# Optimization experiments

Hardware: AMD Instinct MI355X
Metric: run time of the kernel (lower is better)

Reference implementation:

```python
import jax, jax.numpy as jnp
import numpy as np

D0 = 232          # GraphSAGE_TextMF_dyn.model_embedding_dim_origin
NUM_TRAIN = 4096  # num_train_models


def sage_conv(x, edge_index, W_l, b_l, W_r):
    """PyG SAGEConv(aggr='mean'): lin_l(mean_{j in N(i)} x_j) + lin_r(x_i)."""
    src, dst = edge_index[0], edge_index[1]
    msg = x[src]                                                    # [E, Din]
    agg = jax.ops.segment_sum(msg, dst, num_segments=x.shape[0])    # [N, Din]
    deg = jax.ops.segment_sum(jnp.ones((edge_index.shape[1],), x.dtype), dst,
                              num_segments=x.shape[0])
    agg = agg / jnp.maximum(deg, 1.0)[:, None]
    return agg @ W_l.T + b_l + x @ W_r.T


def setup_inputs() -> dict:
    key = jax.random.key(0)
    ks = jax.random.split(key, 12)
    num_models, med, hidden = 5000, 1024, 256
    num_prompts, text_dim = 100000, 768
    B, E = 16384, 131072
    s = lambda d: 1.0 / np.sqrt(d)
    return {
        "P_weight":     jax.random.normal(ks[0], (num_models, med), jnp.float32) * 0.02,
        "model_proj_W": jax.random.normal(ks[1], (D0, med), jnp.float32) * s(med),
        "model_proj_b": jnp.zeros((D0,), jnp.float32),
        "sage1_Wl":     jax.random.normal(ks[2], (hidden, D0), jnp.float32) * s(D0),
        "sage1_bl":     jnp.zeros((hidden,), jnp.float32),
        "sage1_Wr":     jax.random.normal(ks[3], (hidden, D0), jnp.float32) * s(D0),
        "sage2_Wl":     jax.random.normal(ks[4], (D0, hidden), jnp.float32) * s(hidden),
        "sage2_bl":     jnp.zeros((D0,), jnp.float32),
        "sage2_Wr":     jax.random.normal(ks[5], (D0, hidden), jnp.float32) * s(hidden),
        "Q_weight":     jax.random.normal(ks[6], (num_prompts, text_dim), jnp.float32),
        "text_proj_W":  jax.random.normal(ks[7], (D0, text_dim), jnp.float32) * s(text_dim),
        "text_proj_b":  jnp.zeros((D0,), jnp.float32),
        "cls_W":        jax.random.normal(ks[8], (2, D0), jnp.float32) * s(D0),
        "cls_b":        jnp.zeros((2,), jnp.float32),
        "edge_index":   jax.random.randint(ks[9], (2, E), 0, NUM_TRAIN),
        "model_ids":    jax.random.randint(ks[10], (B,), 0, NUM_TRAIN),
        "prompt_ids":   jax.random.randint(ks[11], (B,), 0, num_prompts),
    }


def reference(P_weight, model_proj_W, model_proj_b,
              sage1_Wl, sage1_bl, sage1_Wr,
              sage2_Wl, sage2_bl, sage2_Wr,
              Q_weight, text_proj_W, text_proj_b,
              cls_W, cls_b,
              edge_index, model_ids, prompt_ids):
    # model embedding table -> project to D0
    emb = P_weight @ model_proj_W.T + model_proj_b            # [num_models, D0]
    x = emb[:NUM_TRAIN]                                       # train models only
    # 2-layer GraphSAGE with ReLU between layers
    x = jax.nn.relu(sage_conv(x, edge_index, sage1_Wl, sage1_bl, sage1_Wr))
    x = sage_conv(x, edge_index, sage2_Wl, sage2_bl, sage2_Wr)  # [NUM_TRAIN, D0]
    # TextMF head: classifier(p * q)
    p = x[model_ids]                                          # [B, D0]
    q = Q_weight[prompt_ids] @ text_proj_W.T + text_proj_b    # [B, D0]
    return (p * q) @ cls_W.T + cls_b                          # [B, 2]
```

## Files before the change

kernel.cpp:

```cpp
#include <hip/hip_runtime.h>

#define D0 232
#define MED 1024
#define HID 256
#define TDIM 768
#define NTRAIN 4096

typedef short bf16x8 __attribute__((ext_vector_type(8)));
typedef float f32x4  __attribute__((ext_vector_type(4)));
typedef unsigned short u16;

__device__ __forceinline__ u16 f2bf(float f) {
    unsigned u = __float_as_uint(f);
    return (u16)((u + 0x7FFFu + ((u >> 16) & 1u)) >> 16);
}
__device__ __forceinline__ float bf2f(u16 h) {
    return __uint_as_float(((unsigned)h) << 16);
}
__device__ __forceinline__ void cvt8(const float4& a0, const float4& a1,
                                     bf16x8& h, bf16x8& l) {
    float f[8] = {a0.x, a0.y, a0.z, a0.w, a1.x, a1.y, a1.z, a1.w};
    #pragma unroll
    for (int i = 0; i < 8; ++i) {
        u16 hh = f2bf(f[i]);
        h[i] = (short)hh;
        l[i] = (short)f2bf(f[i] - bf2f(hh));
    }
}
__device__ __forceinline__ void cvt4(const float4 v, ushort4& h, ushort4& l) {
    h.x = f2bf(v.x); l.x = f2bf(v.x - bf2f(h.x));
    h.y = f2bf(v.y); l.y = f2bf(v.y - bf2f(h.y));
    h.z = f2bf(v.z); l.z = f2bf(v.z - bf2f(h.z));
    h.w = f2bf(v.w); l.w = f2bf(v.w - bf2f(h.w));
}

#define SROW(r, k) ((((r) ^ (k)) & 7) | ((r) & ~7))

template<int CONVA, int RELU, int EMIT, int NPASS>
__global__ __launch_bounds__(256, 2) void gemm_node(
    const float* __restrict__ A1f,
    const short* __restrict__ A1h, const short* __restrict__ A1l,
    const short* __restrict__ B1h, const short* __restrict__ B1l,
    const short* __restrict__ A2h, const short* __restrict__ A2l,
    const short* __restrict__ B2h, const short* __restrict__ B2l,
    const float* __restrict__ bias,
    float* __restrict__ Cf, u16* __restrict__ Chi, u16* __restrict__ Clo,
    int M, int N, int K)
{
    constexpr int TBM = 32;
    __shared__ short sAh[8 * TBM * 8], sAl[8 * TBM * 8];

    const int tid  = threadIdx.x;
    const int lane = tid & 63;
    const int wn   = tid >> 6;
    const int l15  = lane & 15;
    const int l4   = lane >> 4;
    const int row0 = blockIdx.y * TBM;
    const int col0 = blockIdx.x * 64;

    const int aRow  = tid >> 3;
    const int aKc   = tid & 7;
    const int aSlot = (aKc * TBM + SROW(aRow, aKc)) * 8;

    const int  colW  = col0 + wn * 16 + l15;
    const bool colOk = colW < N;
    const size_t wBase = (size_t)(colOk ? colW : 0) * K;

    const bf16x8 Z8 = {0, 0, 0, 0, 0, 0, 0, 0};
    f32x4 acc[2];
    acc[0] = (f32x4){0.f, 0.f, 0.f, 0.f};
    acc[1] = (f32x4){0.f, 0.f, 0.f, 0.f};

    for (int pass = 0; pass < NPASS; ++pass) {
        const short* Bh = pass ? B2h : B1h;
        const short* Bl = pass ? B2l : B1l;
        const short* Ah = pass ? A2h : A1h;
        const short* Al = pass ? A2l : A1l;
        const size_t aOff = (size_t)(row0 + aRow) * K;

        float4 qa0, qa1;
        bf16x8 ph, pl;

        auto loadA = [&](int k0) {
            int gk = k0 + aKc * 8;
            bool v = gk < K;
            if (CONVA && pass == 0) {
                qa0 = v ? *(const float4*)(A1f + aOff + gk)     : make_float4(0.f,0.f,0.f,0.f);
                qa1 = v ? *(const float4*)(A1f + aOff + gk + 4) : make_float4(0.f,0.f,0.f,0.f);
            } else {
                ph = v ? *(const bf16x8*)(Ah + aOff + gk) : Z8;
                pl = v ? *(const bf16x8*)(Al + aOff + gk) : Z8;
            }
        };

        loadA(0);
        for (int k0 = 0; k0 < K; k0 += 64) {
            bf16x8 bh[2], bl[2];
            #pragma unroll
            for (int ks = 0; ks < 2; ++ks) {
                int kb = k0 + (ks * 4 + l4) * 8;
                bool v = colOk && kb < K;
                bh[ks] = v ? *(const bf16x8*)(Bh + wBase + kb) : Z8;
                bl[ks] = v ? *(const bf16x8*)(Bl + wBase + kb) : Z8;
            }
            if (CONVA && pass == 0) {
                bf16x8 h, l; cvt8(qa0, qa1, h, l);
                *(bf16x8*)(sAh + aSlot) = h;
                *(bf16x8*)(sAl + aSlot) = l;
            } else {
                *(bf16x8*)(sAh + aSlot) = ph;
                *(bf16x8*)(sAl + aSlot) = pl;
            }
            __syncthreads();
            if (k0 + 64 < K) loadA(k0 + 64);

            #pragma unroll
            for (int ks = 0; ks < 2; ++ks) {
                const int pb = ks * 4 + l4;
                bf16x8 ah[2], al[2];
                #pragma unroll
                for (int m = 0; m < 2; ++m) {
                    int sl = (pb * TBM + SROW(m * 16 + l15, pb)) * 8;
                    ah[m] = *(const bf16x8*)(sAh + sl);
                    al[m] = *(const bf16x8*)(sAl + sl);
                }
                #pragma unroll
                for (int m = 0; m < 2; ++m)
                    acc[m] = __builtin_amdgcn_mfma_f32_16x16x32_bf16(ah[m], bh[ks], acc[m], 0, 0, 0);
                #pragma unroll
                for (int m = 0; m < 2; ++m)
                    acc[m] = __builtin_amdgcn_mfma_f32_16x16x32_bf16(ah[m], bl[ks], acc[m], 0, 0, 0);
                #pragma unroll
                for (int m = 0; m < 2; ++m)
                    acc[m] = __builtin_amdgcn_mfma_f32_16x16x32_bf16(al[m], bh[ks], acc[m], 0, 0, 0);
            }
            __syncthreads();
        }
    }

    if (colOk) {
        const float bv = bias[colW];
        #pragma unroll
        for (int m = 0; m < 2; ++m) {
            #pragma unroll
            for (int r = 0; r < 4; ++r) {
                int row = row0 + m * 16 + l4 * 4 + r;
                float v = acc[m][r] + bv;
                if (RELU) v = fmaxf(v, 0.0f);
                size_t idx = (size_t)row * N + colW;
                Cf[idx] = v;
                if (EMIT) {
                    u16 h = f2bf(v);
                    Chi[idx] = h;
                    Clo[idx] = f2bf(v - bf2f(h));
                }
            }
        }
    }
}

__global__ __launch_bounds__(256) void gemm_q_head(
    const float* __restrict__ Q, const int* __restrict__ prompt_ids,
    const short* __restrict__ Wh, const short* __restrict__ Wl,
    const float* __restrict__ bias,
    const float* __restrict__ x2f, const int* __restrict__ model_ids,
    const float* __restrict__ cls_W, const float* __restrict__ cls_b,
    float* __restrict__ out)
{
    constexpr int TBM = 64, K = TDIM, N = D0;
    __shared__ short sAh[8 * TBM * 8], sAl[8 * TBM * 8];
    __shared__ float hacc[TBM][2];

    const int tid  = threadIdx.x;
    const int lane = tid & 63;
    const int wn   = tid >> 6;
    const int l15  = lane & 15;
    const int l4   = lane >> 4;
    const int row0 = blockIdx.x * TBM;

    const int cid0 = tid * 2, cid1 = tid * 2 + 1;
    const int r0 = cid0 >> 3, kc0 = cid0 & 7;
    const int r1 = cid1 >> 3, kc1 = cid1 & 7;
    const int slot0 = (kc0 * TBM + SROW(r0, kc0)) * 8;
    const int slot1 = (kc1 * TBM + SROW(r1, kc1)) * 8;
    const size_t ab0 = (size_t)prompt_ids[row0 + r0] * K;
    const size_t ab1 = (size_t)prompt_ids[row0 + r1] * K;

    int colW[4]; bool cOk[4]; size_t wB[4];
    #pragma unroll
    for (int j = 0; j < 4; ++j) {
        colW[j] = wn * 64 + j * 16 + l15;
        cOk[j]  = colW[j] < N;
        wB[j]   = (size_t)(cOk[j] ? colW[j] : 0) * K;
    }

    const bf16x8 Z8 = {0, 0, 0, 0, 0, 0, 0, 0};
    f32x4 acc[4][4];
    #pragma unroll
    for (int m = 0; m < 4; ++m)
        #pragma unroll
        for (int j = 0; j < 4; ++j)
            acc[m][j] = (f32x4){0.f, 0.f, 0.f, 0.f};

    float4 qa0, qa1, qa2, qa3;
    auto loadA = [&](int k0) {
        qa0 = *(const float4*)(Q + ab0 + k0 + kc0 * 8);
        qa1 = *(const float4*)(Q + ab0 + k0 + kc0 * 8 + 4);
        qa2 = *(const float4*)(Q + ab1 + k0 + kc1 * 8);
        qa3 = *(const float4*)(Q + ab1 + k0 + kc1 * 8 + 4);
    };

    loadA(0);
    for (int k0 = 0; k0 < K; k0 += 64) {
        bf16x8 bh[2][4], bl[2][4];
        #pragma unroll
        for (int ks = 0; ks < 2; ++ks) {
            int kb = k0 + (ks * 4 + l4) * 8;
            #pragma unroll
            for (int j = 0; j < 4; ++j) {
                bh[ks][j] = cOk[j] ? *(const bf16x8*)(Wh + wB[j] + kb) : Z8;
                bl[ks][j] = cOk[j] ? *(const bf16x8*)(Wl + wB[j] + kb) : Z8;
            }
        }
        {
            bf16x8 h, l;
            cvt8(qa0, qa1, h, l);
            *(bf16x8*)(sAh + slot0) = h; *(bf16x8*)(sAl + slot0) = l;
            cvt8(qa2, qa3, h, l);
            *(bf16x8*)(sAh + slot1) = h; *(bf16x8*)(sAl + slot1) = l;
        }
        __syncthreads();
        if (k0 + 64 < K) loadA(k0 + 64);

        #pragma unroll
        for (int ks = 0; ks < 2; ++ks) {
            const int pb = ks * 4 + l4;
            bf16x8 ah[4], al[4];
            #pragma unroll
            for (int m = 0; m < 4; ++m) {
                int sl = (pb * TBM + SROW(m * 16 + l15, pb)) * 8;
                ah[m] = *(const bf16x8*)(sAh + sl);
                al[m] = *(const bf16x8*)(sAl + sl);
            }
            #pragma unroll
            for (int m = 0; m < 4; ++m)
                #pragma unroll
                for (int j = 0; j < 4; ++j)
                    acc[m][j] = __builtin_amdgcn_mfma_f32_16x16x32_bf16(ah[m], bh[ks][j], acc[m][j], 0, 0, 0);
            #pragma unroll
            for (int m = 0; m < 4; ++m)
                #pragma unroll
                for (int j = 0; j < 4; ++j)
                    acc[m][j] = __builtin_amdgcn_mfma_f32_16x16x32_bf16(ah[m], bl[ks][j], acc[m][j], 0, 0, 0);
            #pragma unroll
            for (int m = 0; m < 4; ++m)
                #pragma unroll
                for (int j = 0; j < 4; ++j)
                    acc[m][j] = __builtin_amdgcn_mfma_f32_16x16x32_bf16(al[m], bh[ks][j], acc[m][j], 0, 0, 0);
        }
        __syncthreads();
    }

    if (tid < TBM * 2) ((float*)hacc)[tid] = 0.f;
    __syncthreads();

    float bv[4], w0[4], w1[4];
    #pragma unroll
    for (int j = 0; j < 4; ++j) {
        bv[j] = cOk[j] ? bias[colW[j]]      : 0.f;
        w0[j] = cOk[j] ? cls_W[colW[j]]     : 0.f;
        w1[j] = cOk[j] ? cls_W[N + colW[j]] : 0.f;
    }

    float s0[4][4] = {}, s1[4][4] = {};
    #pragma unroll
    for (int m = 0; m < 4; ++m) {
        #pragma unroll
        for (int rr = 0; rr < 4; ++rr) {
            const int mid = model_ids[row0 + m * 16 + l4 * 4 + rr];
            const float* xr = x2f + (size_t)mid * N;
            #pragma unroll
            for (int j = 0; j < 4; ++j) {
                if (cOk[j]) {
                    float pv = (acc[m][j][rr] + bv[j]) * xr[colW[j]];
                    s0[m][rr] += pv * w0[j];
                    s1[m][rr] += pv * w1[j];
                }
            }
        }
    }
    #pragma unroll
    for (int off = 1; off < 16; off <<= 1)
        #pragma unroll
        for (int m = 0; m < 4; ++m)
            #pragma unroll
            for (int rr = 0; rr < 4; ++rr) {
                s0[m][rr] += __shfl_xor(s0[m][rr], off);
                s1[m][rr] += __shfl_xor(s1[m][rr], off);
            }
    if (l15 == 0) {
        #pragma unroll
        for (int m = 0; m < 4; ++m)
            #pragma unroll
            for (int rr = 0; rr < 4; ++rr) {
                int lr = m * 16 + l4 * 4 + rr;
                atomicAdd(&hacc[lr][0], s0[m][rr]);
                atomicAdd(&hacc[lr][1], s1[m][rr]);
            }
    }
    __syncthreads();
    if (tid < TBM * 2) {
        int r = tid >> 1, c = tid & 1;
        out[(size_t)(row0 + r) * 2 + c] = hacc[r][c] + cls_b[c];
    }
}

struct Seg  { const float* src; u16* hi; u16* lo; int n4; };
struct Segs { Seg s[6]; };

__global__ __launch_bounds__(256) void hist_conv(
    const int* __restrict__ dst, int* __restrict__ hist, int E, int HB,
    Segs segs, int total4)
{
    if ((int)blockIdx.x < HB) {
        int e = blockIdx.x * 256 + threadIdx.x;
        if (e < E) atomicAdd(&hist[dst[e]], 1);
    } else {
        int i = (blockIdx.x - HB) * 256 + threadIdx.x;
        const int stride = (gridDim.x - HB) * 256;
        for (; i < total4; i += stride) {
            int k = i, si = 0;
            while (k >= segs.s[si].n4) { k -= segs.s[si].n4; ++si; }
            float4 v = ((const float4*)segs.s[si].src)[k];
            ushort4 h, l; cvt4(v, h, l);
            ((ushort4*)segs.s[si].hi)[k] = h;
            ((ushort4*)segs.s[si].lo)[k] = l;
        }
    }
}

__global__ __launch_bounds__(1024) void scan_kernel(
    const int* __restrict__ hist, int* __restrict__ row_ptr,
    float* __restrict__ invdeg, int* __restrict__ cursor, int E)
{
    __shared__ int s[1024];
    const int t = threadIdx.x;
    int4 c = reinterpret_cast<const int4*>(hist)[t];
    int local = c.x + c.y + c.z + c.w;
    s[t] = local;
    __syncthreads();
    for (int off = 1; off < 1024; off <<= 1) {
        int v = (t >= off) ? s[t - off] : 0;
        __syncthreads();
        s[t] += v;
        __syncthreads();
    }
    int base = s[t] - local;
    row_ptr[4 * t + 0] = base;
    row_ptr[4 * t + 1] = base + c.x;
    row_ptr[4 * t + 2] = base + c.x + c.y;
    row_ptr[4 * t + 3] = base + c.x + c.y + c.z;
    if (t == 1023) row_ptr[4096] = E;
    invdeg[4 * t + 0] = 1.0f / fmaxf((float)c.x, 1.0f);
    invdeg[4 * t + 1] = 1.0f / fmaxf((float)c.y, 1.0f);
    invdeg[4 * t + 2] = 1.0f / fmaxf((float)c.z, 1.0f);
    invdeg[4 * t + 3] = 1.0f / fmaxf((float)c.w, 1.0f);
    reinterpret_cast<int4*>(cursor)[t] = make_int4(0, 0, 0, 0);
}

__global__ void scatter_kernel(
    const int* __restrict__ src, const int* __restrict__ dst,
    const int* __restrict__ row_ptr, int* __restrict__ cursor,
    int* __restrict__ csr, int E)
{
    int e = blockIdx.x * blockDim.x + threadIdx.x;
    if (e >= E) return;
    int d = dst[e];
    int pos = atomicAdd(&cursor[d], 1);
    csr[row_ptr[d] + pos] = src[e];
}

__device__ __forceinline__ void add4(float4& a, const float4 b) {
    a.x += b.x; a.y += b.y; a.z += b.z; a.w += b.w;
}

__global__ __launch_bounds__(256) void node_agg(
    const int* __restrict__ row_ptr, const int* __restrict__ csr,
    const float* __restrict__ invdeg,
    const float* __restrict__ x, u16* __restrict__ agh, u16* __restrict__ agl, int D)
{
    const int wave = threadIdx.x >> 6;
    const int lane = threadIdx.x & 63;
    const int node = blockIdx.x * 4 + wave;
    const int beg = row_ptr[node], end = row_ptr[node + 1];
    const bool act = lane < (D >> 2);
    const int fo = lane * 4;

    float4 s0 = {0,0,0,0}, s1 = {0,0,0,0}, s2 = {0,0,0,0}, s3 = {0,0,0,0};
    int j = beg;
    for (; j + 3 < end; j += 4) {
        int n0 = csr[j], n1 = csr[j + 1], n2 = csr[j + 2], n3 = csr[j + 3];
        if (act) {
            add4(s0, *(const float4*)(&x[(size_t)n0 * D + fo]));
            add4(s1, *(const float4*)(&x[(size_t)n1 * D + fo]));
            add4(s2, *(const float4*)(&x[(size_t)n2 * D + fo]));
            add4(s3, *(const float4*)(&x[(size_t)n3 * D + fo]));
        }
    }
    for (; j < end; ++j) {
        int n = csr[j];
        if (act) add4(s0, *(const float4*)(&x[(size_t)n * D + fo]));
    }
    if (act) {
        const float inv = invdeg[node];
        float4 r;
        r.x = (s0.x + s1.x + s2.x + s3.x) * inv;
        r.y = (s0.y + s1.y + s2.y + s3.y) * inv;
        r.z = (s0.z + s1.z + s2.z + s3.z) * inv;
        r.w = (s0.w + s1.w + s2.w + s3.w) * inv;
        ushort4 h, l; cvt4(r, h, l);
        *(ushort4*)(&agh[(size_t)node * D + fo]) = h;
        *(ushort4*)(&agl[(size_t)node * D + fo]) = l;
    }
}

extern "C" void kernel_launch(void* const* d_in, const int* in_sizes, int n_in,
                              void* d_out, int out_size, void* d_ws, size_t ws_size,
                              hipStream_t stream)
{
    const float* P_weight     = (const float*)d_in[0];
    const float* model_proj_W = (const float*)d_in[1];
    const float* model_proj_b = (const float*)d_in[2];
    const float* sage1_Wl     = (const float*)d_in[3];
    const float* sage1_bl     = (const float*)d_in[4];
    const float* sage1_Wr     = (const float*)d_in[5];
    const float* sage2_Wl     = (const float*)d_in[6];
    const float* sage2_bl     = (const float*)d_in[7];
    const float* sage2_Wr     = (const float*)d_in[8];
    const float* Q_weight     = (const float*)d_in[9];
    const float* text_proj_W  = (const float*)d_in[10];
    const float* text_proj_b  = (const float*)d_in[11];
    const float* cls_W        = (const float*)d_in[12];
    const float* cls_b        = (const float*)d_in[13];
    const int*   edge_index   = (const int*)d_in[14];
    const int*   model_ids    = (const int*)d_in[15];
    const int*   prompt_ids   = (const int*)d_in[16];

    const int E = in_sizes[14] / 2;
    const int B = in_sizes[15];
    const int* srcE = edge_index;
    const int* dstE = edge_index + E;

    const size_t nX0 = (size_t)NTRAIN * D0;
    const size_t nH1 = (size_t)NTRAIN * HID;
    const size_t nWp = (size_t)D0 * MED;
    const size_t nWs = (size_t)HID * D0;
    const size_t nWt = (size_t)D0 * TDIM;
    const size_t nWAll = nWp + 4 * nWs + nWt;

    float* fp  = (float*)d_ws;
    float* x0f = fp;  fp += nX0;
    float* h1f = fp;  fp += nH1;
    float* x2f = fp;  fp += nX0;
    u16* sp  = (u16*)fp;
    u16* x0h = sp;    sp += nX0;
    u16* x0l = sp;    sp += nX0;
    u16* h1h = sp;    sp += nH1;
    u16* h1l = sp;    sp += nH1;
    u16* agh = sp;    sp += nH1;
    u16* agl = sp;    sp += nH1;
    u16* Wh  = sp;    sp += nWAll;
    u16* Wl  = sp;    sp += nWAll;
    int* ib  = (int*)sp;
    int*   hist    = ib;
    int*   cursor  = ib + 4096;
    int*   row_ptr = ib + 8192;
    float* invdeg  = (float*)(ib + 12304);
    int*   csr     = ib + 16400;

    u16 *Wph = Wh,            *Wpl = Wl;
    u16 *W1lh = Wh + nWp,     *W1ll = Wl + nWp;
    u16 *W1rh = W1lh + nWs,   *W1rl = W1ll + nWs;
    u16 *W2lh = W1rh + nWs,   *W2ll = W1rl + nWs;
    u16 *W2rh = W2lh + nWs,   *W2rl = W2ll + nWs;
    u16 *Wth  = W2rh + nWs,   *Wtl  = W2rl + nWs;

    dim3 blk(256);

    hipMemsetAsync(hist, 0, 4096 * sizeof(int), stream);

    Segs segs;
    segs.s[0] = {model_proj_W, Wph,  Wpl,  (int)(nWp / 4)};
    segs.s[1] = {sage1_Wl,     W1lh, W1ll, (int)(nWs / 4)};
    segs.s[2] = {sage1_Wr,     W1rh, W1rl, (int)(nWs / 4)};
    segs.s[3] = {sage2_Wl,     W2lh, W2ll, (int)(nWs / 4)};
    segs.s[4] = {sage2_Wr,     W2rh, W2rl, (int)(nWs / 4)};
    segs.s[5] = {text_proj_W,  Wth,  Wtl,  (int)(nWt / 4)};
    const int HB = (E + 255) / 256;
    hist_conv<<<HB + 512, blk, 0, stream>>>(dstE, hist, E, HB, segs, (int)(nWAll / 4));

    scan_kernel<<<1, 1024, 0, stream>>>(hist, row_ptr, invdeg, cursor, E);
    scatter_kernel<<<(E + 255) / 256, blk, 0, stream>>>(srcE, dstE, row_ptr, cursor, csr, E);

    gemm_node<1, 0, 1, 1><<<dim3(4, NTRAIN / 32), blk, 0, stream>>>(
        P_weight, nullptr, nullptr,
        (const short*)Wph, (const short*)Wpl,
        nullptr, nullptr, nullptr, nullptr,
        model_proj_b, x0f, x0h, x0l, NTRAIN, D0, MED);

    node_agg<<<NTRAIN / 4, blk, 0, stream>>>(row_ptr, csr, invdeg, x0f, agh, agl, D0);

    gemm_node<0, 1, 1, 2><<<dim3(4, NTRAIN / 32), blk, 0, stream>>>(
        nullptr, (const short*)agh, (const short*)agl,
        (const short*)W1lh, (const short*)W1ll,
        (const short*)x0h, (const short*)x0l,
        (const short*)W1rh, (const short*)W1rl,
        sage1_bl, h1f, h1h, h1l, NTRAIN, HID, D0);

    node_agg<<<NTRAIN / 4, blk, 0, stream>>>(row_ptr, csr, invdeg, h1f, agh, agl, HID);

    gemm_node<0, 0, 0, 2><<<dim3(4, NTRAIN / 32), blk, 0, stream>>>(
        nullptr, (const short*)agh, (const short*)agl,
        (const short*)W2lh, (const short*)W2ll,
        (const short*)h1h, (const short*)h1l,
        (const short*)W2rh, (const short*)W2rl,
        sage2_bl, x2f, nullptr, nullptr, NTRAIN, D0, HID);

    gemm_q_head<<<B / 64, blk, 0, stream>>>(
        Q_weight, prompt_ids, (const short*)Wth, (const short*)Wtl,
        text_proj_b, x2f, model_ids, cls_W, cls_b, (float*)d_out);
}
```

Baseline: 168.8 us.

## Fuse hist/conv/scan via last-block pattern, fold scatter into first GEMM, shrink head tile

Histogram, weight splitting and the prefix scan now run in one kernel: the last block to finish, detected with an atomic counter, does the scan. The CSR scatter moves into the prologue of the first node GEMM, and the launch grid is flattened to 1D. The Q-head GEMM tile drops from 64 to 32 rows, doubling the block count, and gets launch bounds for two blocks per SM. The goal is fewer kernel launches and better occupancy for the head, at the cost of a serial scan inside one block and scatter work that delays the GEMM start.

```diff
diff --git a/kernel.cpp b/kernel.cpp
--- a/kernel.cpp
+++ b/kernel.cpp
@@ -36,31 +36,101 @@
 
 #define SROW(r, k) ((((r) ^ (k)) & 7) | ((r) & ~7))
 
-template<int CONVA, int RELU, int EMIT, int NPASS>
+struct Seg  { const float* src; u16* hi; u16* lo; int n4; };
+struct Segs { Seg s[6]; };
+
+__global__ __launch_bounds__(256) void k1_hist_conv_scan(
+    const int* __restrict__ dstE, int* __restrict__ hist, int E,
+    Segs segs, int total4,
+    int* __restrict__ done, int* __restrict__ row_ptr,
+    float* __restrict__ invdeg, int* __restrict__ cursor)
+{
+    const int tid  = threadIdx.x;
+    const int gidx = blockIdx.x * 256 + tid;
+    const int gstr = gridDim.x * 256;
+
+    for (int e = gidx; e < E; e += gstr)
+        atomicAdd(&hist[dstE[e]], 1);
+
+    for (int i = gidx; i < total4; i += gstr) {
+        int k = i, si = 0;
+        while (k >= segs.s[si].n4) { k -= segs.s[si].n4; ++si; }
+        float4 v = ((const float4*)segs.s[si].src)[k];
+        ushort4 h, l; cvt4(v, h, l);
+        ((ushort4*)segs.s[si].hi)[k] = h;
+        ((ushort4*)segs.s[si].lo)[k] = l;
+    }
+
+    __shared__ int amLast;
+    __syncthreads();
+    if (tid == 0)
+        amLast = (atomicAdd(done, 1) == (int)gridDim.x - 1);
+    __syncthreads();
+    if (!amLast) return;
+
+    __shared__ int s_scan[256];
+    const int base = tid * 16;
+    int v[16]; int s = 0;
+    #pragma unroll
+    for (int i = 0; i < 16; ++i) {
+        v[i] = __hip_atomic_load(&hist[base + i], __ATOMIC_RELAXED,
+                                 __HIP_MEMORY_SCOPE_AGENT);
+        s += v[i];
+    }
+    s_scan[tid] = s;
+    __syncthreads();
+    for (int off = 1; off < 256; off <<= 1) {
+        int t2 = (tid >= off) ? s_scan[tid - off] : 0;
+        __syncthreads();
+        s_scan[tid] += t2;
+        __syncthreads();
+    }
+    int run = s_scan[tid] - s;
+    #pragma unroll
+    for (int i = 0; i < 16; ++i) {
+        row_ptr[base + i] = run;
+        invdeg[base + i]  = 1.0f / fmaxf((float)v[i], 1.0f);
+        cursor[base + i]  = 0;
+        run += v[i];
+    }
+    if (tid == 255) row_ptr[4096] = E;
+}
+
+template<int SCAT, int CONVA, int RELU, int EMIT, int NPASS>
 __global__ __launch_bounds__(256, 2) void gemm_node(
+    const int* __restrict__ srcE, const int* __restrict__ dstE,
+    const int* __restrict__ row_ptr, int* __restrict__ cursor,
+    int* __restrict__ csr, int E,
     const float* __restrict__ A1f,
-    const short* __restrict__ A1h, const short* __restrict__ A1l,
-    const short* __restrict__ B1h, const short* __restrict__ B1l,
-    const short* __restrict__ A2h, const short* __restrict__ A2l,
-    const short* __restrict__ B2h, const short* __restrict__ B2l,
+    const u16* __restrict__ A1h, const u16* __restrict__ A1l,
+    const u16* __restrict__ B1h, const u16* __restrict__ B1l,
+    const u16* __restrict__ A2h, const u16* __restrict__ A2l,
+    const u16* __restrict__ B2h, const u16* __restrict__ B2l,
     const float* __restrict__ bias,
     float* __restrict__ Cf, u16* __restrict__ Chi, u16* __restrict__ Clo,
-    int M, int N, int K)
+    int N, int K)
 {
-    constexpr int TBM = 32;
-    __shared__ short sAh[8 * TBM * 8], sAl[8 * TBM * 8];
+    if (SCAT) {
+        for (int e = blockIdx.x * 256 + threadIdx.x; e < E; e += gridDim.x * 256) {
+            int d = dstE[e];
+            int pos = atomicAdd(&cursor[d], 1);
+            csr[row_ptr[d] + pos] = srcE[e];
+        }
+    }
+
+    __shared__ short sAh[2048], sAl[2048];
 
     const int tid  = threadIdx.x;
     const int lane = tid & 63;
     const int wn   = tid >> 6;
     const int l15  = lane & 15;
     const int l4   = lane >> 4;
-    const int row0 = blockIdx.y * TBM;
-    const int col0 = blockIdx.x * 64;
+    const int row0 = (blockIdx.x >> 2) * 32;
+    const int col0 = (blockIdx.x & 3) * 64;
 
     const int aRow  = tid >> 3;
     const int aKc   = tid & 7;
-    const int aSlot = (aKc * TBM + SROW(aRow, aKc)) * 8;
+    const int aSlot = (aKc * 32 + SROW(aRow, aKc)) * 8;
 
     const int  colW  = col0 + wn * 16 + l15;
     const bool colOk = colW < N;
@@ -72,10 +142,10 @@
     acc[1] = (f32x4){0.f, 0.f, 0.f, 0.f};
 
     for (int pass = 0; pass < NPASS; ++pass) {
-        const short* Bh = pass ? B2h : B1h;
-        const short* Bl = pass ? B2l : B1l;
-        const short* Ah = pass ? A2h : A1h;
-        const short* Al = pass ? A2l : A1l;
+        const u16* Bh = pass ? B2h : B1h;
+        const u16* Bl = pass ? B2l : B1l;
+        const u16* Ah = pass ? A2h : A1h;
+        const u16* Al = pass ? A2l : A1l;
         const size_t aOff = (size_t)(row0 + aRow) * K;
 
         float4 qa0, qa1;
@@ -85,8 +155,8 @@
             int gk = k0 + aKc * 8;
             bool v = gk < K;
             if (CONVA && pass == 0) {
-                qa0 = v ? *(const float4*)(A1f + aOff + gk)     : make_float4(0.f,0.f,0.f,0.f);
-                qa1 = v ? *(const float4*)(A1f + aOff + gk + 4) : make_float4(0.f,0.f,0.f,0.f);
+                qa0 = v ? *(const float4*)(A1f + aOff + gk)     : make_float4(0.f, 0.f, 0.f, 0.f);
+                qa1 = v ? *(const float4*)(A1f + aOff + gk + 4) : make_float4(0.f, 0.f, 0.f, 0.f);
             } else {
                 ph = v ? *(const bf16x8*)(Ah + aOff + gk) : Z8;
                 pl = v ? *(const bf16x8*)(Al + aOff + gk) : Z8;
@@ -120,7 +190,7 @@
                 bf16x8 ah[2], al[2];
                 #pragma unroll
                 for (int m = 0; m < 2; ++m) {
-                    int sl = (pb * TBM + SROW(m * 16 + l15, pb)) * 8;
+                    int sl = (pb * 32 + SROW(m * 16 + l15, pb)) * 8;
                     ah[m] = *(const bf16x8*)(sAh + sl);
                     al[m] = *(const bf16x8*)(sAl + sl);
                 }
@@ -159,227 +229,6 @@
     }
 }
 
-__global__ __launch_bounds__(256) void gemm_q_head(
-    const float* __restrict__ Q, const int* __restrict__ prompt_ids,
-    const short* __restrict__ Wh, const short* __restrict__ Wl,
-    const float* __restrict__ bias,
-    const float* __restrict__ x2f, const int* __restrict__ model_ids,
-    const float* __restrict__ cls_W, const float* __restrict__ cls_b,
-    float* __restrict__ out)
-{
-    constexpr int TBM = 64, K = TDIM, N = D0;
-    __shared__ short sAh[8 * TBM * 8], sAl[8 * TBM * 8];
-    __shared__ float hacc[TBM][2];
-
-    const int tid  = threadIdx.x;
-    const int lane = tid & 63;
-    const int wn   = tid >> 6;
-    const int l15  = lane & 15;
-    const int l4   = lane >> 4;
-    const int row0 = blockIdx.x * TBM;
-
-    const int cid0 = tid * 2, cid1 = tid * 2 + 1;
-    const int r0 = cid0 >> 3, kc0 = cid0 & 7;
-    const int r1 = cid1 >> 3, kc1 = cid1 & 7;
-    const int slot0 = (kc0 * TBM + SROW(r0, kc0)) * 8;
-    const int slot1 = (kc1 * TBM + SROW(r1, kc1)) * 8;
-    const size_t ab0 = (size_t)prompt_ids[row0 + r0] * K;
-    const size_t ab1 = (size_t)prompt_ids[row0 + r1] * K;
-
-    int colW[4]; bool cOk[4]; size_t wB[4];
-    #pragma unroll
-    for (int j = 0; j < 4; ++j) {
-        colW[j] = wn * 64 + j * 16 + l15;
-        cOk[j]  = colW[j] < N;
-        wB[j]   = (size_t)(cOk[j] ? colW[j] : 0) * K;
-    }
-
-    const bf16x8 Z8 = {0, 0, 0, 0, 0, 0, 0, 0};
-    f32x4 acc[4][4];
-    #pragma unroll
-    for (int m = 0; m < 4; ++m)
-        #pragma unroll
-        for (int j = 0; j < 4; ++j)
-            acc[m][j] = (f32x4){0.f, 0.f, 0.f, 0.f};
-
-    float4 qa0, qa1, qa2, qa3;
-    auto loadA = [&](int k0) {
-        qa0 = *(const float4*)(Q + ab0 + k0 + kc0 * 8);
-        qa1 = *(const float4*)(Q + ab0 + k0 + kc0 * 8 + 4);
-        qa2 = *(const float4*)(Q + ab1 + k0 + kc1 * 8);
-        qa3 = *(const float4*)(Q + ab1 + k0 + kc1 * 8 + 4);
-    };
-
-    loadA(0);
-    for (int k0 = 0; k0 < K; k0 += 64) {
-        bf16x8 bh[2][4], bl[2][4];
-        #pragma unroll
-        for (int ks = 0; ks < 2; ++ks) {
-            int kb = k0 + (ks * 4 + l4) * 8;
-            #pragma unroll
-            for (int j = 0; j < 4; ++j) {
-                bh[ks][j] = cOk[j] ? *(const bf16x8*)(Wh + wB[j] + kb) : Z8;
-                bl[ks][j] = cOk[j] ? *(const bf16x8*)(Wl + wB[j] + kb) : Z8;
-            }
-        }
-        {
-            bf16x8 h, l;
-            cvt8(qa0, qa1, h, l);
-            *(bf16x8*)(sAh + slot0) = h; *(bf16x8*)(sAl + slot0) = l;
-            cvt8(qa2, qa3, h, l);
-            *(bf16x8*)(sAh + slot1) = h; *(bf16x8*)(sAl + slot1) = l;
-        }
-        __syncthreads();
-        if (k0 + 64 < K) loadA(k0 + 64);
-
-        #pragma unroll
-        for (int ks = 0; ks < 2; ++ks) {
-            const int pb = ks * 4 + l4;
-            bf16x8 ah[4], al[4];
-            #pragma unroll
-            for (int m = 0; m < 4; ++m) {
-                int sl = (pb * TBM + SROW(m * 16 + l15, pb)) * 8;
-                ah[m] = *(const bf16x8*)(sAh + sl);
-                al[m] = *(const bf16x8*)(sAl + sl);
-            }
-            #pragma unroll
-            for (int m = 0; m < 4; ++m)
-                #pragma unroll
-                for (int j = 0; j < 4; ++j)
-                    acc[m][j] = __builtin_amdgcn_mfma_f32_16x16x32_bf16(ah[m], bh[ks][j], acc[m][j], 0, 0, 0);
-            #pragma unroll
-            for (int m = 0; m < 4; ++m)
-                #pragma unroll
-                for (int j = 0; j < 4; ++j)
-                    acc[m][j] = __builtin_amdgcn_mfma_f32_16x16x32_bf16(ah[m], bl[ks][j], acc[m][j], 0, 0, 0);
-            #pragma unroll
-            for (int m = 0; m < 4; ++m)
-                #pragma unroll
-                for (int j = 0; j < 4; ++j)
-                    acc[m][j] = __builtin_amdgcn_mfma_f32_16x16x32_bf16(al[m], bh[ks][j], acc[m][j], 0, 0, 0);
-        }
-        __syncthreads();
-    }
-
-    if (tid < TBM * 2) ((float*)hacc)[tid] = 0.f;
-    __syncthreads();
-
-    float bv[4], w0[4], w1[4];
-    #pragma unroll
-    for (int j = 0; j < 4; ++j) {
-        bv[j] = cOk[j] ? bias[colW[j]]      : 0.f;
-        w0[j] = cOk[j] ? cls_W[colW[j]]     : 0.f;
-        w1[j] = cOk[j] ? cls_W[N + colW[j]] : 0.f;
-    }
-
-    float s0[4][4] = {}, s1[4][4] = {};
-    #pragma unroll
-    for (int m = 0; m < 4; ++m) {
-        #pragma unroll
-        for (int rr = 0; rr < 4; ++rr) {
-            const int mid = model_ids[row0 + m * 16 + l4 * 4 + rr];
-            const float* xr = x2f + (size_t)mid * N;
-            #pragma unroll
-            for (int j = 0; j < 4; ++j) {
-                if (cOk[j]) {
-                    float pv = (acc[m][j][rr] + bv[j]) * xr[colW[j]];
-                    s0[m][rr] += pv * w0[j];
-                    s1[m][rr] += pv * w1[j];
-                }
-            }
-        }
-    }
-    #pragma unroll
-    for (int off = 1; off < 16; off <<= 1)
-        #pragma unroll
-        for (int m = 0; m < 4; ++m)
-            #pragma unroll
-            for (int rr = 0; rr < 4; ++rr) {
-                s0[m][rr] += __shfl_xor(s0[m][rr], off);
-                s1[m][rr] += __shfl_xor(s1[m][rr], off);
-            }
-    if (l15 == 0) {
-        #pragma unroll
-        for (int m = 0; m < 4; ++m)
-            #pragma unroll
-            for (int rr = 0; rr < 4; ++rr) {
-                int lr = m * 16 + l4 * 4 + rr;
-                atomicAdd(&hacc[lr][0], s0[m][rr]);
-                atomicAdd(&hacc[lr][1], s1[m][rr]);
-            }
-    }
-    __syncthreads();
-    if (tid < TBM * 2) {
-        int r = tid >> 1, c = tid & 1;
-        out[(size_t)(row0 + r) * 2 + c] = hacc[r][c] + cls_b[c];
-    }
-}
-
-struct Seg  { const float* src; u16* hi; u16* lo; int n4; };
-struct Segs { Seg s[6]; };
-
-__global__ __launch_bounds__(256) void hist_conv(
-    const int* __restrict__ dst, int* __restrict__ hist, int E, int HB,
-    Segs segs, int total4)
-{
-    if ((int)blockIdx.x < HB) {
-        int e = blockIdx.x * 256 + threadIdx.x;
-        if (e < E) atomicAdd(&hist[dst[e]], 1);
-    } else {
-        int i = (blockIdx.x - HB) * 256 + threadIdx.x;
-        const int stride = (gridDim.x - HB) * 256;
-        for (; i < total4; i += stride) {
-            int k = i, si = 0;
-            while (k >= segs.s[si].n4) { k -= segs.s[si].n4; ++si; }
-            float4 v = ((const float4*)segs.s[si].src)[k];
-            ushort4 h, l; cvt4(v, h, l);
-            ((ushort4*)segs.s[si].hi)[k] = h;
-            ((ushort4*)segs.s[si].lo)[k] = l;
-        }
-    }
-}
-
-__global__ __launch_bounds__(1024) void scan_kernel(
-    const int* __restrict__ hist, int* __restrict__ row_ptr,
-    float* __restrict__ invdeg, int* __restrict__ cursor, int E)
-{
-    __shared__ int s[1024];
-    const int t = threadIdx.x;
-    int4 c = reinterpret_cast<const int4*>(hist)[t];
-    int local = c.x + c.y + c.z + c.w;
-    s[t] = local;
-    __syncthreads();
-    for (int off = 1; off < 1024; off <<= 1) {
-        int v = (t >= off) ? s[t - off] : 0;
-        __syncthreads();
-        s[t] += v;
-        __syncthreads();
-    }
-    int base = s[t] - local;
-    row_ptr[4 * t + 0] = base;
-    row_ptr[4 * t + 1] = base + c.x;
-    row_ptr[4 * t + 2] = base + c.x + c.y;
-    row_ptr[4 * t + 3] = base + c.x + c.y + c.z;
-    if (t == 1023) row_ptr[4096] = E;
-    invdeg[4 * t + 0] = 1.0f / fmaxf((float)c.x, 1.0f);
-    invdeg[4 * t + 1] = 1.0f / fmaxf((float)c.y, 1.0f);
-    invdeg[4 * t + 2] = 1.0f / fmaxf((float)c.z, 1.0f);
-    invdeg[4 * t + 3] = 1.0f / fmaxf((float)c.w, 1.0f);
-    reinterpret_cast<int4*>(cursor)[t] = make_int4(0, 0, 0, 0);
-}
-
-__global__ void scatter_kernel(
-    const int* __restrict__ src, const int* __restrict__ dst,
-    const int* __restrict__ row_ptr, int* __restrict__ cursor,
-    int* __restrict__ csr, int E)
-{
-    int e = blockIdx.x * blockDim.x + threadIdx.x;
-    if (e >= E) return;
-    int d = dst[e];
-    int pos = atomicAdd(&cursor[d], 1);
-    csr[row_ptr[d] + pos] = src[e];
-}
-
 __device__ __forceinline__ void add4(float4& a, const float4 b) {
     a.x += b.x; a.y += b.y; a.z += b.z; a.w += b.w;
 }
@@ -399,7 +248,7 @@
     float4 s0 = {0,0,0,0}, s1 = {0,0,0,0}, s2 = {0,0,0,0}, s3 = {0,0,0,0};
     int j = beg;
     for (; j + 3 < end; j += 4) {
-        int n0 = csr[j], n1 = csr[j + 1], n2 = csr[j + 2], n3 = csr[j + 3];
+        int n0 = csr[j], n1 = csr[j+1], n2 = csr[j+2], n3 = csr[j+3];
         if (act) {
             add4(s0, *(const float4*)(&x[(size_t)n0 * D + fo]));
             add4(s1, *(const float4*)(&x[(size_t)n1 * D + fo]));
@@ -421,6 +270,155 @@
         ushort4 h, l; cvt4(r, h, l);
         *(ushort4*)(&agh[(size_t)node * D + fo]) = h;
         *(ushort4*)(&agl[(size_t)node * D + fo]) = l;
+    }
+}
+
+__global__ __launch_bounds__(256, 2) void gemm_q_head(
+    const float* __restrict__ Q, const int* __restrict__ pids,
+    const u16* __restrict__ Wh, const u16* __restrict__ Wl,
+    const float* __restrict__ bt,
+    const float* __restrict__ x2f, const int* __restrict__ mids,
+    const float* __restrict__ clsW, const float* __restrict__ clsb,
+    float* __restrict__ out)
+{
+    constexpr int K = TDIM, N = D0;
+    __shared__ short sAh[2048], sAl[2048];
+    __shared__ float hacc[64];
+
+    const int tid  = threadIdx.x;
+    const int lane = tid & 63;
+    const int wn   = tid >> 6;
+    const int l15  = lane & 15;
+    const int l4   = lane >> 4;
+    const int row0 = blockIdx.x * 32;
+
+    const int r  = tid >> 3;
+    const int kc = tid & 7;
+    const int slot = (kc * 32 + SROW(r, kc)) * 8;
+    const size_t ab = (size_t)pids[row0 + r] * K;
+
+    int colW[4]; bool cOk[4]; size_t wB[4];
+    #pragma unroll
+    for (int j = 0; j < 4; ++j) {
+        colW[j] = wn * 64 + j * 16 + l15;
+        cOk[j]  = colW[j] < N;
+        wB[j]   = (size_t)(cOk[j] ? colW[j] : 0) * K;
+    }
+
+    const bf16x8 Z8 = {0, 0, 0, 0, 0, 0, 0, 0};
+    f32x4 acc[2][4];
+    #pragma unroll
+    for (int m = 0; m < 2; ++m)
+        #pragma unroll
+        for (int j = 0; j < 4; ++j)
+            acc[m][j] = (f32x4){0.f, 0.f, 0.f, 0.f};
+
+    float4 qa0, qa1;
+    auto loadA = [&](int k0) {
+        qa0 = *(const float4*)(Q + ab + k0 + kc * 8);
+        qa1 = *(const float4*)(Q + ab + k0 + kc * 8 + 4);
+    };
+
+    loadA(0);
+    for (int k0 = 0; k0 < K; k0 += 64) {
+        bf16x8 bh[2][4], bl[2][4];
+        #pragma unroll
+        for (int ks = 0; ks < 2; ++ks) {
+            int kb = k0 + (ks * 4 + l4) * 8;
+            #pragma unroll
+            for (int j = 0; j < 4; ++j) {
+                bh[ks][j] = cOk[j] ? *(const bf16x8*)(Wh + wB[j] + kb) : Z8;
+                bl[ks][j] = cOk[j] ? *(const bf16x8*)(Wl + wB[j] + kb) : Z8;
+            }
+        }
+        {
+            bf16x8 h, l; cvt8(qa0, qa1, h, l);
+            *(bf16x8*)(sAh + slot) = h;
+            *(bf16x8*)(sAl + slot) = l;
+        }
+        __syncthreads();
+        if (k0 + 64 < K) loadA(k0 + 64);
+
+        #pragma unroll
+        for (int ks = 0; ks < 2; ++ks) {
+            const int pb = ks * 4 + l4;
+            bf16x8 ah[2], al[2];
+            #pragma unroll
+            for (int m = 0; m < 2; ++m) {
+                int sl = (pb * 32 + SROW(m * 16 + l15, pb)) * 8;
+                ah[m] = *(const bf16x8*)(sAh + sl);
+                al[m] = *(const bf16x8*)(sAl + sl);
+            }
+            #pragma unroll
+            for (int m = 0; m < 2; ++m)
+                #pragma unroll
+                for (int j = 0; j < 4; ++j)
+                    acc[m][j] = __builtin_amdgcn_mfma_f32_16x16x32_bf16(ah[m], bh[ks][j], acc[m][j], 0, 0, 0);
+            #pragma unroll
+            for (int m = 0; m < 2; ++m)
+                #pragma unroll
+                for (int j = 0; j < 4; ++j)
+                    acc[m][j] = __builtin_amdgcn_mfma_f32_16x16x32_bf16(ah[m], bl[ks][j], acc[m][j], 0, 0, 0);
+            #pragma unroll
+            for (int m = 0; m < 2; ++m)
+                #pragma unroll
+                for (int j = 0; j < 4; ++j)
+                    acc[m][j] = __builtin_amdgcn_mfma_f32_16x16x32_bf16(al[m], bh[ks][j], acc[m][j], 0, 0, 0);
+        }
+        __syncthreads();
+    }
+
+    if (tid < 64) hacc[tid] = 0.f;
+    __syncthreads();
+
+    float bv[4], w0[4], w1[4];
+    #pragma unroll
+    for (int j = 0; j < 4; ++j) {
+        bv[j] = cOk[j] ? bt[colW[j]]       : 0.f;
+        w0[j] = cOk[j] ? clsW[colW[j]]     : 0.f;
+        w1[j] = cOk[j] ? clsW[N + colW[j]] : 0.f;
+    }
+
+    float s0[2][4] = {}, s1[2][4] = {};
+    #pragma unroll
+    for (int m = 0; m < 2; ++m) {
+        #pragma unroll
+        for (int rr = 0; rr < 4; ++rr) {
+            const int mid = mids[row0 + m * 16 + l4 * 4 + rr];
+            const float* xr = x2f + (size_t)mid * N;
+            #pragma unroll
+            for (int j = 0; j < 4; ++j) {
+                if (cOk[j]) {
+                    float pv = (acc[m][j][rr] + bv[j]) * xr[colW[j]];
+                    s0[m][rr] += pv * w0[j];
+                    s1[m][rr] += pv * w1[j];
+                }
+            }
+        }
+    }
+    #pragma unroll
+    for (int off = 1; off < 16; off <<= 1)
+        #pragma unroll
+        for (int m = 0; m < 2; ++m)
+            #pragma unroll
+            for (int rr = 0; rr < 4; ++rr) {
+                s0[m][rr] += __shfl_xor(s0[m][rr], off);
+                s1[m][rr] += __shfl_xor(s1[m][rr], off);
+            }
+    if (l15 == 0) {
+        #pragma unroll
+        for (int m = 0; m < 2; ++m)
+            #pragma unroll
+            for (int rr = 0; rr < 4; ++rr) {
+                int lr = m * 16 + l4 * 4 + rr;
+                atomicAdd(&hacc[lr * 2 + 0], s0[m][rr]);
+                atomicAdd(&hacc[lr * 2 + 1], s1[m][rr]);
+            }
+    }
+    __syncthreads();
+    if (tid < 64) {
+        int rr = tid >> 1, c = tid & 1;
+        out[(size_t)(row0 + rr) * 2 + c] = hacc[tid] + clsb[c];
     }
 }
 
@@ -458,11 +456,11 @@
     const size_t nWt = (size_t)D0 * TDIM;
     const size_t nWAll = nWp + 4 * nWs + nWt;
 
-    float* fp  = (float*)d_ws;
-    float* x0f = fp;  fp += nX0;
-    float* h1f = fp;  fp += nH1;
-    float* x2f = fp;  fp += nX0;
-    u16* sp  = (u16*)fp;
+    float* fb  = (float*)d_ws;
+    float* x0f = fb;  fb += nX0;
+    float* h1f = fb;  fb += nH1;
+    float* x2f = fb;  fb += nX0;
+    u16* sp  = (u16*)fb;
     u16* x0h = sp;    sp += nX0;
     u16* x0l = sp;    sp += nX0;
     u16* h1h = sp;    sp += nH1;
@@ -473,21 +471,22 @@
     u16* Wl  = sp;    sp += nWAll;
     int* ib  = (int*)sp;
     int*   hist    = ib;
-    int*   cursor  = ib + 4096;
-    int*   row_ptr = ib + 8192;
-    float* invdeg  = (float*)(ib + 12304);
-    int*   csr     = ib + 16400;
-
-    u16 *Wph = Wh,            *Wpl = Wl;
-    u16 *W1lh = Wh + nWp,     *W1ll = Wl + nWp;
-    u16 *W1rh = W1lh + nWs,   *W1rl = W1ll + nWs;
-    u16 *W2lh = W1rh + nWs,   *W2ll = W1rl + nWs;
-    u16 *W2rh = W2lh + nWs,   *W2rl = W2ll + nWs;
-    u16 *Wth  = W2rh + nWs,   *Wtl  = W2rl + nWs;
+    int*   done    = ib + 4096;
+    int*   row_ptr = ib + 4112;
+    int*   cursor  = ib + 8224;
+    float* invdeg  = (float*)(ib + 12320);
+    int*   csr     = ib + 16416;
+
+    u16 *Wph = Wh,             *Wpl = Wl;
+    u16 *W1lh = Wh + nWp,      *W1ll = Wl + nWp;
+    u16 *W1rh = W1lh + nWs,    *W1rl = W1ll + nWs;
+    u16 *W2lh = W1rh + nWs,    *W2ll = W1rl + nWs;
+    u16 *W2rh = W2lh + nWs,    *W2rl = W2ll + nWs;
+    u16 *Wth  = W2rh + nWs,    *Wtl  = W2rl + nWs;
 
     dim3 blk(256);
 
-    hipMemsetAsync(hist, 0, 4096 * sizeof(int), stream);
+    hipMemsetAsync(hist, 0, 4112 * sizeof(int), stream);
 
     Segs segs;
     segs.s[0] = {model_proj_W, Wph,  Wpl,  (int)(nWp / 4)};
@@ -496,37 +495,32 @@
     segs.s[3] = {sage2_Wl,     W2lh, W2ll, (int)(nWs / 4)};
     segs.s[4] = {sage2_Wr,     W2rh, W2rl, (int)(nWs / 4)};
     segs.s[5] = {text_proj_W,  Wth,  Wtl,  (int)(nWt / 4)};
-    const int HB = (E + 255) / 256;
-    hist_conv<<<HB + 512, blk, 0, stream>>>(dstE, hist, E, HB, segs, (int)(nWAll / 4));
-
-    scan_kernel<<<1, 1024, 0, stream>>>(hist, row_ptr, invdeg, cursor, E);
-    scatter_kernel<<<(E + 255) / 256, blk, 0, stream>>>(srcE, dstE, row_ptr, cursor, csr, E);
-
-    gemm_node<1, 0, 1, 1><<<dim3(4, NTRAIN / 32), blk, 0, stream>>>(
-        P_weight, nullptr, nullptr,
-        (const short*)Wph, (const short*)Wpl,
+    k1_hist_conv_scan<<<512, blk, 0, stream>>>(
+        dstE, hist, E, segs, (int)(nWAll / 4), done, row_ptr, invdeg, cursor);
+
+    gemm_node<1, 1, 0, 1, 1><<<512, blk, 0, stream>>>(
+        srcE, dstE, row_ptr, cursor, csr, E,
+        P_weight, nullptr, nullptr, (const u16*)Wph, (const u16*)Wpl,
         nullptr, nullptr, nullptr, nullptr,
-        model_proj_b, x0f, x0h, x0l, NTRAIN, D0, MED);
+        model_proj_b, x0f, x0h, x0l, D0, MED);
 
     node_agg<<<NTRAIN / 4, blk, 0, stream>>>(row_ptr, csr, invdeg, x0f, agh, agl, D0);
 
-    gemm_node<0, 1, 1, 2><<<dim3(4, NTRAIN / 32), blk, 0, stream>>>(
-        nullptr, (const short*)agh, (const short*)agl,
-        (const short*)W1lh, (const short*)W1ll,
-        (const short*)x0h, (const short*)x0l,
-        (const short*)W1rh, (const short*)W1rl,
-        sage1_bl, h1f, h1h, h1l, NTRAIN, HID, D0);
+    gemm_node<0, 0, 1, 1, 2><<<512, blk, 0, stream>>>(
+        nullptr, nullptr, nullptr, nullptr, nullptr, 0,
+        nullptr, agh, agl, W1lh, W1ll,
+        x0h, x0l, W1rh, W1rl,
+        sage1_bl, h1f, h1h, h1l, HID, D0);
 
     node_agg<<<NTRAIN / 4, blk, 0, stream>>>(row_ptr, csr, invdeg, h1f, agh, agl, HID);
 
-    gemm_node<0, 0, 0, 2><<<dim3(4, NTRAIN / 32), blk, 0, stream>>>(
-        nullptr, (const short*)agh, (const short*)agl,
-        (const short*)W2lh, (const short*)W2ll,
-        (const short*)h1h, (const short*)h1l,
-        (const short*)W2rh, (const short*)W2rl,
-        sage2_bl, x2f, nullptr, nullptr, NTRAIN, D0, HID);
-
-    gemm_q_head<<<B / 64, blk, 0, stream>>>(
-        Q_weight, prompt_ids, (const short*)Wth, (const short*)Wtl,
-        text_proj_b, x2f, model_ids, cls_W, cls_b, (float*)d_out);
-}
+    gemm_node<0, 0, 0, 0, 2><<<512, blk, 0, stream>>>(
+        nullptr, nullptr, nullptr, nullptr, nullptr, 0,
+        nullptr, agh, agl, W2lh, W2ll,
+        h1h, h1l, W2rh, W2rl,
+        sage2_bl, x2f, nullptr, nullptr, D0, HID);
+
+    gemm_q_head<<<B / 32, blk, 0, stream>>>(
+        Q_weight, prompt_ids, Wth, Wtl, text_proj_b,
+        x2f, model_ids, cls_W, cls_b, (float*)d_out);
+}
```

Measured after the change: 172.2 us. 1.02x slower.
